# Kernel optimization log

Measured on AMD Instinct MI355X. Metric: run time of the kernel, lower is better.

## Reference

```python
import jax, jax.numpy as jnp
import numpy as np

N, E, D, H, L, G = 50000, 640000, 128, 128, 3, 1024
EPS = 1e-5


def setup_inputs() -> dict:
    key = jax.random.key(0)
    k1, k2, k3, k4 = jax.random.split(key, 4)
    x = jax.random.normal(k1, (N, D), dtype=jnp.float32)
    Ws = jax.random.normal(k2, (L, D, H), dtype=jnp.float32) * (1.0 / np.sqrt(D))
    bs = jnp.zeros((L, H), dtype=jnp.float32)
    gammas = jnp.ones((L, H), dtype=jnp.float32)
    betas = jnp.zeros((L, H), dtype=jnp.float32)
    edge_index = jax.random.randint(k3, (2, E), 0, N, dtype=jnp.int32)
    batch_idx = jnp.sort(jax.random.randint(k4, (N,), 0, G, dtype=jnp.int32))
    return {"x": x, "Ws": Ws, "bs": bs, "gammas": gammas, "betas": betas,
            "edge_index": edge_index, "batch_idx": batch_idx, "num_graphs": G}


def reference(x, Ws, bs, gammas, betas, edge_index, batch_idx, num_graphs):
    n = x.shape[0]
    loop = jnp.arange(n, dtype=edge_index.dtype)
    src = jnp.concatenate([edge_index[0], loop])  # [E+N] with self loops
    dst = jnp.concatenate([edge_index[1], loop])
    # symmetric GCN normalization: deg computed at destinations (incl self loops)
    deg = jax.ops.segment_sum(jnp.ones_like(dst, dtype=x.dtype), dst, num_segments=n)
    dinv = jnp.where(deg > 0, jax.lax.rsqrt(deg), 0.0)
    norm = (dinv[src] * dinv[dst])[:, None]  # [E+N, 1]

    h = x
    for l in range(L):
        h = h @ Ws[l]                                         # [N, H]
        msg = norm * h[src]                                   # gather  [E+N, H]
        h = jax.ops.segment_sum(msg, dst, num_segments=n) + bs[l]  # scatter-add
        mu = jnp.mean(h, axis=0)
        var = jnp.mean((h - mu) ** 2, axis=0)                 # biased var (BN)
        h = gammas[l] * (h - mu) * jax.lax.rsqrt(var + EPS) + betas[l]
        h = jax.nn.elu(h)
        # dropout: eval mode -> identity

    sums = jax.ops.segment_sum(h, batch_idx, num_segments=num_graphs)   # [G, H]
    counts = jax.ops.segment_sum(jnp.ones((n,), dtype=h.dtype), batch_idx,
                                 num_segments=num_graphs)
    return sums / jnp.maximum(counts, 1.0)[:, None]
```

## Files before the change

### kernel.cpp

```cpp
#include <hip/hip_runtime.h>
#include <hip/hip_fp16.h>
#include <math.h>

#define NN 50000
#define EE 640000
#define DD 128
#define LL 3
#define GGR 1024
#define NBLK 196

typedef _Float16 half8 __attribute__((ext_vector_type(8)));
typedef float f32x4 __attribute__((ext_vector_type(4)));

__global__ __launch_bounds__(256) void k_hist(const int* __restrict__ dst,
                                              int* __restrict__ cnt) {
  int e = blockIdx.x * 256 + threadIdx.x;
  if (e < EE) atomicAdd(&cnt[dst[e]], 1);
}

__global__ __launch_bounds__(256) void k_scan1(const int* __restrict__ cnt,
                                               int* __restrict__ part) {
  int i = blockIdx.x * 256 + threadIdx.x;
  int v = (i < NN) ? cnt[i] : 0;
  __shared__ int red[256];
  red[threadIdx.x] = v;
  __syncthreads();
  for (int off = 128; off > 0; off >>= 1) {
    if (threadIdx.x < off) red[threadIdx.x] += red[threadIdx.x + off];
    __syncthreads();
  }
  if (threadIdx.x == 0) part[blockIdx.x] = red[0];
}

__global__ __launch_bounds__(256) void k_scan2(int* __restrict__ part,
                                               float* __restrict__ stats) {
  stats[threadIdx.x] = 0.0f;
  stats[256 + threadIdx.x] = 0.0f;
  stats[512 + threadIdx.x] = 0.0f;
  __shared__ int a[256];
  int t = threadIdx.x;
  int own = (t < NBLK) ? part[t] : 0;
  a[t] = own;
  __syncthreads();
  for (int off = 1; off < 256; off <<= 1) {
    int v = (t >= off) ? a[t - off] : 0;
    __syncthreads();
    a[t] += v;
    __syncthreads();
  }
  if (t < NBLK) part[t] = a[t] - own;
}

__global__ __launch_bounds__(256) void k_scan3(const int* __restrict__ cnt,
                                               const int* __restrict__ part,
                                               int* __restrict__ rowstart,
                                               int* __restrict__ cursor,
                                               float* __restrict__ dinv) {
  int t = threadIdx.x;
  int i = blockIdx.x * 256 + t;
  int c = (i < NN) ? cnt[i] : 0;
  __shared__ int a[256];
  a[t] = c;
  __syncthreads();
  for (int off = 1; off < 256; off <<= 1) {
    int v = (t >= off) ? a[t - off] : 0;
    __syncthreads();
    a[t] += v;
    __syncthreads();
  }
  int excl = a[t] - c + part[blockIdx.x];
  if (i < NN) {
    rowstart[i] = excl;
    cursor[i] = excl;
    dinv[i] = rsqrtf((float)(c + 1));
  }
  if (i == 0) rowstart[NN] = EE;
}

__global__ __launch_bounds__(256) void k_scatter(const int* __restrict__ src,
                                                 const int* __restrict__ dst,
                                                 int* __restrict__ cursor,
                                                 int* __restrict__ csr_src) {
  int e = blockIdx.x * 256 + threadIdx.x;
  if (e < EE) {
    int pos = atomicAdd(&cursor[dst[e]], 1);
    csr_src[pos] = src[e];
  }
}

__global__ __launch_bounds__(256) void k_wprep(const float* __restrict__ Ws,
                                               __half* __restrict__ Wth,
                                               __half* __restrict__ Wtl) {
  int i = blockIdx.x * 256 + threadIdx.x;
  if (i >= LL * DD * DD) return;
  int l = i >> 14;
  int rem = i & 16383;
  int k = rem >> 7, col = rem & 127;
  float w = Ws[i];
  __half hi = __float2half(w);
  __half lo = __float2half(w - __half2float(hi));
  size_t o = (size_t)l * DD * DD + (size_t)col * DD + k;
  Wth[o] = hi;
  Wtl[o] = lo;
}

__device__ __forceinline__ float elu1(float x) {
  return x > 0.0f ? x : expm1f(x);
}

template <int ACT>
__global__ __launch_bounds__(512) void k_gemm(const void* __restrict__ Xin,
                                              const __half* __restrict__ Wth,
                                              const __half* __restrict__ Wtl,
                                              __half* __restrict__ Yh,
                                              const float* __restrict__ stats,
                                              const float* __restrict__ gamma_,
                                              const float* __restrict__ beta_,
                                              const float* __restrict__ dinv) {
  __shared__ __align__(16) __half Wh_s[DD * DD];
  __shared__ __align__(16) __half Wl_s[DD * DD];
  __shared__ __align__(16) __half Xh_s[128 * DD];
  __shared__ __align__(16) __half Xl_s[128 * DD];
  __shared__ float scs[DD], shs[DD];
  const int t = threadIdx.x;
  if (ACT && t < DD) {
    float mu = stats[t] * (1.0f / NN);
    float var = stats[DD + t] * (1.0f / NN) - mu * mu;
    float rsig = rsqrtf(var + 1e-5f);
    float sc = gamma_[t] * rsig;
    scs[t] = sc;
    shs[t] = beta_[t] - sc * mu;
  }
  char* WhB = (char*)Wh_s;
  char* WlB = (char*)Wl_s;
  for (int ch = t; ch < DD * DD / 8; ch += 512) {
    int col = ch >> 4;
    int k0 = (ch & 15) << 3;
    half8 h = *reinterpret_cast<const half8*>(Wth + (size_t)col * DD + k0);
    half8 l = *reinterpret_cast<const half8*>(Wtl + (size_t)col * DD + k0);
    int off = col * 256 + ((k0 * 2) ^ ((col & 7) << 4));
    *reinterpret_cast<half8*>(WhB + off) = h;
    *reinterpret_cast<half8*>(WlB + off) = l;
  }
  __syncthreads();

  const int base = blockIdx.x * 128;
  char* XhB = (char*)Xh_s;
  char* XlB = (char*)Xl_s;
  for (int i = t; i < 128 * 32; i += 512) {
    int rl = i >> 5;
    int r = base + rl;
    int kq = i & 31;
    float4 v = make_float4(0.f, 0.f, 0.f, 0.f);
    float dv = 0.0f;
    if (r < NN) {
      if (ACT) {
        const __half2* X2 = reinterpret_cast<const __half2*>(Xin);
        float2 p0 = __half22float2(X2[(size_t)r * 64 + kq * 2]);
        float2 p1 = __half22float2(X2[(size_t)r * 64 + kq * 2 + 1]);
        v = make_float4(p0.x, p0.y, p1.x, p1.y);
      } else {
        v = reinterpret_cast<const float4*>(Xin)[(size_t)r * 32 + kq];
      }
      dv = dinv[r];
    }
    if (ACT) {
      float4 sc = reinterpret_cast<const float4*>(scs)[kq];
      float4 sh = reinterpret_cast<const float4*>(shs)[kq];
      v.x = elu1(fmaf(v.x, sc.x, sh.x));
      v.y = elu1(fmaf(v.y, sc.y, sh.y));
      v.z = elu1(fmaf(v.z, sc.z, sh.z));
      v.w = elu1(fmaf(v.w, sc.w, sh.w));
    }
    v.x *= dv; v.y *= dv; v.z *= dv; v.w *= dv;
    __half2 h0 = __floats2half2_rn(v.x, v.y);
    __half2 h1 = __floats2half2_rn(v.z, v.w);
    __half2 l0 = __floats2half2_rn(v.x - __low2float(h0), v.y - __high2float(h0));
    __half2 l1 = __floats2half2_rn(v.z - __low2float(h1), v.w - __high2float(h1));
    int off = rl * 256 + ((kq * 8) ^ ((rl & 7) << 4));
    *reinterpret_cast<__half2*>(XhB + off) = h0;
    *reinterpret_cast<__half2*>(XhB + off + 4) = h1;
    *reinterpret_cast<__half2*>(XlB + off) = l0;
    *reinterpret_cast<__half2*>(XlB + off + 4) = l1;
  }
  __syncthreads();

  const int w = t >> 6, l = t & 63;
  const int lr = l & 15, lg = l >> 4;
  const int arow = w * 16 + lr;
  const int aswz = (arow & 7) << 4;
  f32x4 acc[8];
#pragma unroll
  for (int c = 0; c < 8; ++c) acc[c] = (f32x4){0.f, 0.f, 0.f, 0.f};
#pragma unroll
  for (int kk = 0; kk < 4; ++kk) {
    int kbyte = kk * 64 + lg * 16;
    half8 Ah = *reinterpret_cast<half8*>(XhB + arow * 256 + (kbyte ^ aswz));
    half8 Al = *reinterpret_cast<half8*>(XlB + arow * 256 + (kbyte ^ aswz));
#pragma unroll
    for (int c = 0; c < 8; ++c) {
      int col = c * 16 + lr;
      int boff = col * 256 + (kbyte ^ ((col & 7) << 4));
      half8 Bh = *reinterpret_cast<half8*>(WhB + boff);
      half8 Bl = *reinterpret_cast<half8*>(WlB + boff);
      acc[c] = __builtin_amdgcn_mfma_f32_16x16x32_f16(Ah, Bh, acc[c], 0, 0, 0);
      acc[c] = __builtin_amdgcn_mfma_f32_16x16x32_f16(Al, Bh, acc[c], 0, 0, 0);
      acc[c] = __builtin_amdgcn_mfma_f32_16x16x32_f16(Ah, Bl, acc[c], 0, 0, 0);
    }
  }
#pragma unroll
  for (int c = 0; c < 8; ++c) {
#pragma unroll
    for (int j = 0; j < 4; ++j) {
      int row = base + w * 16 + lg * 4 + j;
      if (row < NN)
        Yh[(size_t)row * DD + c * 16 + lr] = __float2half(acc[c][j]);
    }
  }
}

__global__ __launch_bounds__(256) void k_agg_csr(const __half2* __restrict__ Hs,
                                                 const int* __restrict__ rowstart,
                                                 const int* __restrict__ csr_src,
                                                 const float* __restrict__ dinv,
                                                 __half2* __restrict__ outh) {
  int d = blockIdx.x * 4 + (threadIdx.x >> 6);
  if (d >= NN) return;
  int lane = threadIdx.x & 63;
  int beg = rowstart[d], end = rowstart[d + 1];

  float2 s = __half22float2(Hs[(size_t)d * 64 + lane]);
  float ax0 = s.x, ay0 = s.y;
  float ax1 = 0.f, ay1 = 0.f, ax2 = 0.f, ay2 = 0.f, ax3 = 0.f, ay3 = 0.f;

  for (int i = beg; i < end; i += 8) {
    float2 v[8];
#pragma unroll
    for (int j = 0; j < 8; ++j) {
      int sj = csr_src[min(i + j, end - 1)];
      v[j] = __half22float2(Hs[(size_t)sj * 64 + lane]);
    }
#pragma unroll
    for (int j = 0; j < 8; ++j) {
      bool ok = (i + j < end);
      float wx = ok ? v[j].x : 0.f;
      float wy = ok ? v[j].y : 0.f;
      switch (j & 3) {
        case 0: ax0 += wx; ay0 += wy; break;
        case 1: ax1 += wx; ay1 += wy; break;
        case 2: ax2 += wx; ay2 += wy; break;
        default: ax3 += wx; ay3 += wy; break;
      }
    }
  }
  float dv = dinv[d];
  float rx = (ax0 + ax1 + ax2 + ax3) * dv;
  float ry = (ay0 + ay1 + ay2 + ay3) * dv;
  outh[(size_t)d * 64 + lane] = __floats2half2_rn(rx, ry);
}

__global__ __launch_bounds__(256) void k_bnstats(const __half2* __restrict__ H,
                                                 float* __restrict__ stats) {
  int g = threadIdx.x >> 6;
  int lane = threadIdx.x & 63;
  float sx = 0.f, sy = 0.f, qx = 0.f, qy = 0.f;
  for (int r = blockIdx.x * 4 + g; r < NN; r += 256 * 4) {
    float2 v = __half22float2(H[(size_t)r * 64 + lane]);
    sx += v.x; sy += v.y;
    qx = fmaf(v.x, v.x, qx);
    qy = fmaf(v.y, v.y, qy);
  }
  __shared__ float reds[4][128];
  __shared__ float redq[4][128];
  reds[g][2 * lane] = sx; reds[g][2 * lane + 1] = sy;
  redq[g][2 * lane] = qx; redq[g][2 * lane + 1] = qy;
  __syncthreads();
  int t = threadIdx.x;
  if (t < 128) {
    float s = reds[0][t] + reds[1][t] + reds[2][t] + reds[3][t];
    float q = redq[0][t] + redq[1][t] + redq[2][t] + redq[3][t];
    atomicAdd(&stats[t], s);
    atomicAdd(&stats[DD + t], q);
  }
}

__global__ __launch_bounds__(256) void k_pool(const __half* __restrict__ H,
                                              const int* __restrict__ bidx,
                                              const float* __restrict__ stats,
                                              const float* __restrict__ gamma_,
                                              const float* __restrict__ beta_,
                                              float* __restrict__ out,
                                              float* __restrict__ cnts) {
  __shared__ float scs[DD], shs[DD];
  int f = threadIdx.x & 127;
  int h = threadIdx.x >> 7;
  if (threadIdx.x < DD) {
    float mu = stats[threadIdx.x] * (1.0f / NN);
    float var = stats[DD + threadIdx.x] * (1.0f / NN) - mu * mu;
    float rsig = rsqrtf(var + 1e-5f);
    float sc = gamma_[threadIdx.x] * rsig;
    scs[threadIdx.x] = sc;
    shs[threadIdx.x] = beta_[threadIdx.x] - sc * mu;
  }
  __syncthreads();
  int n0 = blockIdx.x * 128 + h * 64;
  if (n0 >= NN) return;
  int n1 = min(n0 + 64, NN);
  float sc = scs[f], sh = shs[f];
  int gcur = bidx[n0];
  float racc = 0.0f, rcnt = 0.0f;
  for (int n = n0; n < n1; ++n) {
    int g = bidx[n];
    if (g != gcur) {
      atomicAdd(&out[(size_t)gcur * DD + f], racc);
      if (f == 0) atomicAdd(&cnts[gcur], rcnt);
      gcur = g;
      racc = 0.0f;
      rcnt = 0.0f;
    }
    float v = elu1(fmaf(__half2float(H[(size_t)n * DD + f]), sc, sh));
    racc += v;
    rcnt += 1.0f;
  }
  atomicAdd(&out[(size_t)gcur * DD + f], racc);
  if (f == 0) atomicAdd(&cnts[gcur], rcnt);
}

__global__ __launch_bounds__(256) void k_div(float* __restrict__ out,
                                             const float* __restrict__ cnts) {
  int i = blockIdx.x * 256 + threadIdx.x;
  if (i >= GGR * DD) return;
  out[i] = out[i] / fmaxf(cnts[i >> 7], 1.0f);
}

extern "C" void kernel_launch(void* const* d_in, const int* in_sizes, int n_in,
                              void* d_out, int out_size, void* d_ws, size_t ws_size,
                              hipStream_t stream) {
  const float* x      = (const float*)d_in[0];
  const float* Ws     = (const float*)d_in[1];
  const float* gammas = (const float*)d_in[3];
  const float* betas  = (const float*)d_in[4];
  const int*   ei     = (const int*)d_in[5];
  const int*   bidx   = (const int*)d_in[6];
  const int* srcp = ei;
  const int* dstp = ei + EE;

  __half* Wth  = (__half*)d_ws;
  __half* Wtl  = Wth + (size_t)LL * DD * DD;
  __half* bufA = (__half*)(Wtl + (size_t)LL * DD * DD);
  __half* bufB = bufA + (size_t)NN * DD;
  float* dinv  = (float*)(bufB + (size_t)NN * DD);
  float* stats = dinv + NN;
  float* cnts  = stats + 3 * 256;
  int* cnt      = (int*)(cnts + GGR);
  int* rowstart = cnt + NN;
  int* cursor   = rowstart + NN + 1;
  int* csr_src  = cursor + NN;
  int* part     = csr_src + EE;
  float* out = (float*)d_out;

  k_wprep<<<(LL * DD * DD + 255) / 256, 256, 0, stream>>>(Ws, Wth, Wtl);

  hipMemsetAsync(cnt, 0, NN * sizeof(int), stream);
  k_hist<<<(EE + 255) / 256, 256, 0, stream>>>(dstp, cnt);
  k_scan1<<<NBLK, 256, 0, stream>>>(cnt, part);
  k_scan2<<<1, 256, 0, stream>>>(part, stats);
  k_scan3<<<NBLK, 256, 0, stream>>>(cnt, part, rowstart, cursor, dinv);
  k_scatter<<<(EE + 255) / 256, 256, 0, stream>>>(srcp, dstp, cursor, csr_src);

  const void* Xin = x;
  for (int l = 0; l < LL; ++l) {
    const __half* Wh = Wth + (size_t)l * DD * DD;
    const __half* Wl = Wtl + (size_t)l * DD * DD;
    if (l == 0)
      k_gemm<0><<<(NN + 127) / 128, 512, 0, stream>>>(
          Xin, Wh, Wl, bufB, stats, gammas, betas, dinv);
    else
      k_gemm<1><<<(NN + 127) / 128, 512, 0, stream>>>(
          Xin, Wh, Wl, bufB, stats + (l - 1) * 256, gammas + (l - 1) * DD,
          betas + (l - 1) * DD, dinv);
    k_agg_csr<<<(NN + 3) / 4, 256, 0, stream>>>((const __half2*)bufB, rowstart,
                                                csr_src, dinv, (__half2*)bufA);
    k_bnstats<<<256, 256, 0, stream>>>((const __half2*)bufA, stats + l * 256);
    Xin = bufA;
  }

  hipMemsetAsync(out, 0, (size_t)GGR * DD * sizeof(float), stream);
  hipMemsetAsync(cnts, 0, GGR * sizeof(float), stream);
  k_pool<<<(NN + 127) / 128, 256, 0, stream>>>(bufA, bidx, stats + 2 * 256,
                                               gammas + 2 * DD, betas + 2 * DD,
                                               out, cnts);
  k_div<<<(GGR * DD + 255) / 256, 256, 0, stream>>>(out, cnts);
}
```

Baseline: 391.9 us.

## Merge setup kernels, fold memsets into scan, load GEMM A operand directly

```diff
diff --git a/kernel.cpp b/kernel.cpp
--- a/kernel.cpp
+++ b/kernel.cpp
@@ -12,14 +12,38 @@
 typedef _Float16 half8 __attribute__((ext_vector_type(8)));
 typedef float f32x4 __attribute__((ext_vector_type(4)));
 
-__global__ __launch_bounds__(256) void k_hist(const int* __restrict__ dst,
+__global__ __launch_bounds__(256) void k_prep(const float* __restrict__ Ws,
+                                              __half* __restrict__ Wth,
+                                              __half* __restrict__ Wtl,
+                                              const int* __restrict__ dst,
                                               int* __restrict__ cnt) {
-  int e = blockIdx.x * 256 + threadIdx.x;
-  if (e < EE) atomicAdd(&cnt[dst[e]], 1);
+  int b = blockIdx.x;
+  if (b < 192) {
+    int i = b * 256 + threadIdx.x;
+    int l = i >> 14;
+    int rem = i & 16383;
+    int k = rem >> 7, col = rem & 127;
+    float w = Ws[i];
+    __half hi = __float2half(w);
+    __half lo = __float2half(w - __half2float(hi));
+    size_t o = (size_t)l * DD * DD + (size_t)col * DD + k;
+    Wth[o] = hi;
+    Wtl[o] = lo;
+  } else {
+    int e = (b - 192) * 256 + threadIdx.x;
+    if (e < EE) atomicAdd(&cnt[dst[e]], 1);
+  }
 }
 
 __global__ __launch_bounds__(256) void k_scan1(const int* __restrict__ cnt,
-                                               int* __restrict__ part) {
+                                               int* __restrict__ part,
+                                               float* __restrict__ out,
+                                               float* __restrict__ cnts) {
+  for (int i = blockIdx.x * 256 + threadIdx.x; i < GGR * DD + GGR;
+       i += NBLK * 256) {
+    if (i < GGR * DD) out[i] = 0.0f;
+    else cnts[i - GGR * DD] = 0.0f;
+  }
   int i = blockIdx.x * 256 + threadIdx.x;
   int v = (i < NN) ? cnt[i] : 0;
   __shared__ int red[256];
@@ -86,22 +110,6 @@
     int pos = atomicAdd(&cursor[dst[e]], 1);
     csr_src[pos] = src[e];
   }
-}
-
-__global__ __launch_bounds__(256) void k_wprep(const float* __restrict__ Ws,
-                                               __half* __restrict__ Wth,
-                                               __half* __restrict__ Wtl) {
-  int i = blockIdx.x * 256 + threadIdx.x;
-  if (i >= LL * DD * DD) return;
-  int l = i >> 14;
-  int rem = i & 16383;
-  int k = rem >> 7, col = rem & 127;
-  float w = Ws[i];
-  __half hi = __float2half(w);
-  __half lo = __float2half(w - __half2float(hi));
-  size_t o = (size_t)l * DD * DD + (size_t)col * DD + k;
-  Wth[o] = hi;
-  Wtl[o] = lo;
 }
 
 __device__ __forceinline__ float elu1(float x) {
@@ -119,8 +127,6 @@
                                               const float* __restrict__ dinv) {
   __shared__ __align__(16) __half Wh_s[DD * DD];
   __shared__ __align__(16) __half Wl_s[DD * DD];
-  __shared__ __align__(16) __half Xh_s[128 * DD];
-  __shared__ __align__(16) __half Xl_s[128 * DD];
   __shared__ float scs[DD], shs[DD];
   const int t = threadIdx.x;
   if (ACT && t < DD) {
@@ -133,7 +139,7 @@
   }
   char* WhB = (char*)Wh_s;
   char* WlB = (char*)Wl_s;
-  for (int ch = t; ch < DD * DD / 8; ch += 512) {
+  for (int ch = t; ch < DD * 16; ch += 512) {
     int col = ch >> 4;
     int k0 = (ch & 15) << 3;
     half8 h = *reinterpret_cast<const half8*>(Wth + (size_t)col * DD + k0);
@@ -145,58 +151,54 @@
   __syncthreads();
 
   const int base = blockIdx.x * 128;
-  char* XhB = (char*)Xh_s;
-  char* XlB = (char*)Xl_s;
-  for (int i = t; i < 128 * 32; i += 512) {
-    int rl = i >> 5;
-    int r = base + rl;
-    int kq = i & 31;
-    float4 v = make_float4(0.f, 0.f, 0.f, 0.f);
-    float dv = 0.0f;
-    if (r < NN) {
-      if (ACT) {
-        const __half2* X2 = reinterpret_cast<const __half2*>(Xin);
-        float2 p0 = __half22float2(X2[(size_t)r * 64 + kq * 2]);
-        float2 p1 = __half22float2(X2[(size_t)r * 64 + kq * 2 + 1]);
-        v = make_float4(p0.x, p0.y, p1.x, p1.y);
-      } else {
-        v = reinterpret_cast<const float4*>(Xin)[(size_t)r * 32 + kq];
-      }
-      dv = dinv[r];
-    }
-    if (ACT) {
-      float4 sc = reinterpret_cast<const float4*>(scs)[kq];
-      float4 sh = reinterpret_cast<const float4*>(shs)[kq];
-      v.x = elu1(fmaf(v.x, sc.x, sh.x));
-      v.y = elu1(fmaf(v.y, sc.y, sh.y));
-      v.z = elu1(fmaf(v.z, sc.z, sh.z));
-      v.w = elu1(fmaf(v.w, sc.w, sh.w));
-    }
-    v.x *= dv; v.y *= dv; v.z *= dv; v.w *= dv;
-    __half2 h0 = __floats2half2_rn(v.x, v.y);
-    __half2 h1 = __floats2half2_rn(v.z, v.w);
-    __half2 l0 = __floats2half2_rn(v.x - __low2float(h0), v.y - __high2float(h0));
-    __half2 l1 = __floats2half2_rn(v.z - __low2float(h1), v.w - __high2float(h1));
-    int off = rl * 256 + ((kq * 8) ^ ((rl & 7) << 4));
-    *reinterpret_cast<__half2*>(XhB + off) = h0;
-    *reinterpret_cast<__half2*>(XhB + off + 4) = h1;
-    *reinterpret_cast<__half2*>(XlB + off) = l0;
-    *reinterpret_cast<__half2*>(XlB + off + 4) = l1;
-  }
-  __syncthreads();
-
   const int w = t >> 6, l = t & 63;
   const int lr = l & 15, lg = l >> 4;
-  const int arow = w * 16 + lr;
-  const int aswz = (arow & 7) << 4;
+  const int grow = base + w * 16 + lr;
+  const bool rok = grow < NN;
+  const int growc = rok ? grow : NN - 1;
+  const float dv = rok ? dinv[growc] : 0.0f;
+
   f32x4 acc[8];
 #pragma unroll
   for (int c = 0; c < 8; ++c) acc[c] = (f32x4){0.f, 0.f, 0.f, 0.f};
+
 #pragma unroll
   for (int kk = 0; kk < 4; ++kk) {
-    int kbyte = kk * 64 + lg * 16;
-    half8 Ah = *reinterpret_cast<half8*>(XhB + arow * 256 + (kbyte ^ aswz));
-    half8 Al = *reinterpret_cast<half8*>(XlB + arow * 256 + (kbyte ^ aswz));
+    const int kbase = kk * 32 + lg * 8;
+    float xv[8];
+    if (ACT) {
+      half8 raw = *reinterpret_cast<const half8*>(
+          (const __half*)Xin + (size_t)growc * DD + kbase);
+#pragma unroll
+      for (int j = 0; j < 8; ++j) xv[j] = (float)raw[j];
+      float4 sc0 = *reinterpret_cast<const float4*>(&scs[kbase]);
+      float4 sc1 = *reinterpret_cast<const float4*>(&scs[kbase + 4]);
+      float4 sh0 = *reinterpret_cast<const float4*>(&shs[kbase]);
+      float4 sh1 = *reinterpret_cast<const float4*>(&shs[kbase + 4]);
+      xv[0] = elu1(fmaf(xv[0], sc0.x, sh0.x));
+      xv[1] = elu1(fmaf(xv[1], sc0.y, sh0.y));
+      xv[2] = elu1(fmaf(xv[2], sc0.z, sh0.z));
+      xv[3] = elu1(fmaf(xv[3], sc0.w, sh0.w));
+      xv[4] = elu1(fmaf(xv[4], sc1.x, sh1.x));
+      xv[5] = elu1(fmaf(xv[5], sc1.y, sh1.y));
+      xv[6] = elu1(fmaf(xv[6], sc1.z, sh1.z));
+      xv[7] = elu1(fmaf(xv[7], sc1.w, sh1.w));
+    } else {
+      const float4* Xf = reinterpret_cast<const float4*>(Xin);
+      float4 a = Xf[(size_t)growc * 32 + (kbase >> 2)];
+      float4 b = Xf[(size_t)growc * 32 + (kbase >> 2) + 1];
+      xv[0] = a.x; xv[1] = a.y; xv[2] = a.z; xv[3] = a.w;
+      xv[4] = b.x; xv[5] = b.y; xv[6] = b.z; xv[7] = b.w;
+    }
+    half8 Ah, Al;
+#pragma unroll
+    for (int j = 0; j < 8; ++j) {
+      float s = xv[j] * dv;
+      _Float16 h = (_Float16)s;
+      Ah[j] = h;
+      Al[j] = (_Float16)(s - (float)h);
+    }
+    const int kbyte = kk * 64 + lg * 16;
 #pragma unroll
     for (int c = 0; c < 8; ++c) {
       int col = c * 16 + lr;
@@ -359,11 +361,9 @@
   int* part     = csr_src + EE;
   float* out = (float*)d_out;
 
-  k_wprep<<<(LL * DD * DD + 255) / 256, 256, 0, stream>>>(Ws, Wth, Wtl);
-
   hipMemsetAsync(cnt, 0, NN * sizeof(int), stream);
-  k_hist<<<(EE + 255) / 256, 256, 0, stream>>>(dstp, cnt);
-  k_scan1<<<NBLK, 256, 0, stream>>>(cnt, part);
+  k_prep<<<192 + (EE + 255) / 256, 256, 0, stream>>>(Ws, Wth, Wtl, dstp, cnt);
+  k_scan1<<<NBLK, 256, 0, stream>>>(cnt, part, out, cnts);
   k_scan2<<<1, 256, 0, stream>>>(part, stats);
   k_scan3<<<NBLK, 256, 0, stream>>>(cnt, part, rowstart, cursor, dinv);
   k_scatter<<<(EE + 255) / 256, 256, 0, stream>>>(srcp, dstp, cursor, csr_src);
@@ -385,8 +385,6 @@
     Xin = bufA;
   }
 
-  hipMemsetAsync(out, 0, (size_t)GGR * DD * sizeof(float), stream);
-  hipMemsetAsync(cnts, 0, GGR * sizeof(float), stream);
   k_pool<<<(NN + 127) / 128, 256, 0, stream>>>(bufA, bidx, stats + 2 * 256,
                                                gammas + 2 * DD, betas + 2 * DD,
                                                out, cnts);
```

New measurement: 366.1 us. 6.6% less time.
